# Kernel tuning notes

Measured on AMD Instinct MI355X. Metric: run time of the kernel, lower is better.

## Reference

```python
import jax, jax.numpy as jnp
import numpy as np

ALPHA = 32.0
LN_EPS = 1e-5

def _cdist(a, b):
    # a: [C, M, K], b: [C, N, K] -> [C, M, N] euclidean distances
    d2 = (jnp.sum(a * a, -1)[:, :, None]
          + jnp.sum(b * b, -1)[:, None, :]
          - 2.0 * jnp.einsum('cmk,cnk->cmn', a, b))
    return jnp.sqrt(jnp.maximum(d2, 1e-12))

def setup_inputs() -> dict:
    key = jax.random.key(0)
    k1, k2 = jax.random.split(key)
    B, D, H, W, C = 8, 16, 28, 28, 256
    CN, SS = 128, 28 * 28
    x = jax.random.normal(k1, (B, D, H, W, C), dtype=jnp.float32)
    ln_weight = jnp.ones((C,), dtype=jnp.float32)
    ln_bias = jnp.zeros((C,), dtype=jnp.float32)
    cluster_center = jax.random.uniform(k2, (C, CN, SS), dtype=jnp.float32)
    return {"x": x, "ln_weight": ln_weight, "ln_bias": ln_bias,
            "cluster_center": cluster_center}

def reference(x, ln_weight, ln_bias, cluster_center):
    B, D, H, W, C = x.shape
    CN = cluster_center.shape[1]
    # LayerNorm over last dim (feature_dim)
    mu = jnp.mean(x, -1, keepdims=True)
    var = jnp.mean(jnp.square(x - mu), -1, keepdims=True)
    xn = (x - mu) * jax.lax.rsqrt(var + LN_EPS) * ln_weight + ln_bias
    # B D H W C -> C (B D) (H W)
    x_re = jnp.transpose(xn, (4, 0, 1, 2, 3)).reshape(C, B * D, H * W)
    soft_assign = _cdist(x_re, cluster_center)          # [C, B*D, CN]
    # C (B D) CN -> B D C CN
    x_distance = jnp.transpose(soft_assign.reshape(C, B, D, CN), (1, 2, 0, 3))
    # NegSoftAssign: exp(-alpha*(x - min)) normalized == softmax(-alpha*x)
    x_distance_assign = jax.nn.softmax(-ALPHA * x_distance, axis=-1)
    cluster_dist = _cdist(cluster_center, cluster_center)  # [C, CN, CN]
    return (x_distance, x_distance_assign, cluster_dist)
```

## Files before the change

### kernel.cpp

```cpp
#include <hip/hip_runtime.h>
#include <hip/hip_bf16.h>
#include <math.h>

#define C_DIM 256
#define BD    128
#define HW    784
#define CN    128
#define KPAD  800

typedef short bf16x8 __attribute__((ext_vector_type(8)));
typedef float f32x4 __attribute__((ext_vector_type(4)));

__device__ inline ushort f2b(float f) {
  unsigned u = __float_as_uint(f);
  unsigned r = (u + 0x7FFFu + ((u >> 16) & 1u)) >> 16;
  return (ushort)r;
}

__global__ __launch_bounds__(256) void ln_transpose_kernel(
    const float* __restrict__ x, const float* __restrict__ lnw,
    const float* __restrict__ lnb, ushort* __restrict__ xre,
    float* __restrict__ anorm) {
  const int HT = 56, LD = 257;
  __shared__ float tile[HT * LD];
  __shared__ float sW[256], sB[256];
  __shared__ float nbuf[4][256];
  int t = threadIdx.x, bd = blockIdx.y, hw0 = blockIdx.x * HT;
  sW[t] = lnw[t]; sB[t] = lnb[t];
  const float* xb = x + ((size_t)bd * HW + hw0) * 256;
  for (int r = 0; r < HT; ++r) tile[r * LD + t] = xb[r * 256 + t];
  __syncthreads();
  int w = t >> 6, lane = t & 63;
  float nrm[4] = {0.f, 0.f, 0.f, 0.f};
  for (int r = w; r < HT; r += 4) {
    float v[4]; float s = 0.f;
    for (int j = 0; j < 4; ++j) { v[j] = tile[r * LD + lane + j * 64]; s += v[j]; }
    for (int off = 32; off >= 1; off >>= 1) s += __shfl_xor(s, off, 64);
    float mu = s * (1.0f / 256.0f);
    float s2 = 0.f;
    for (int j = 0; j < 4; ++j) { float dv = v[j] - mu; s2 += dv * dv; }
    for (int off = 32; off >= 1; off >>= 1) s2 += __shfl_xor(s2, off, 64);
    float scale = rsqrtf(s2 * (1.0f / 256.0f) + 1e-5f);
    for (int j = 0; j < 4; ++j) {
      int c = lane + j * 64;
      float y = (v[j] - mu) * scale * sW[c] + sB[c];
      tile[r * LD + c] = y;
      nrm[j] = fmaf(y, y, nrm[j]);
    }
  }
  for (int j = 0; j < 4; ++j) nbuf[w][lane + j * 64] = nrm[j];
  __syncthreads();
  if (lane < HT) {
    for (int i = 0; i < 64; ++i) {
      int c = i * 4 + w;
      xre[(size_t)c * (BD * KPAD) + (size_t)bd * KPAD + hw0 + lane] =
          f2b(tile[lane * LD + c]);
    }
  } else if (blockIdx.x == 13) {
    int p = lane - 56;
    for (int i = 0; i < 64; ++i) {
      int c = i * 4 + w;
      *(ushort2*)(xre + (size_t)c * (BD * KPAD) + (size_t)bd * KPAD + 784 + p * 2) =
          make_ushort2(0, 0);
    }
  }
  float tot = nbuf[0][t] + nbuf[1][t] + nbuf[2][t] + nbuf[3][t];
  atomicAdd(&anorm[t * 128 + bd], tot);
}

__global__ __launch_bounds__(256) void cc_convert_kernel(
    const float* __restrict__ cc, ushort* __restrict__ ccb,
    float* __restrict__ bnorm) {
  int b = blockIdx.x, c = b >> 2;
  int t = threadIdx.x, w = t >> 6, lane = t & 63;
  int r0 = (b & 3) * 32 + w * 8;
  for (int it = 0; it < 8; ++it) {
    int r = r0 + it;
    const float4* src = (const float4*)(cc + ((size_t)c * CN + r) * HW);
    ushort* dst = ccb + (size_t)c * (CN * KPAD) + (size_t)r * KPAD;
    float nrm = 0.f;
    for (int f = lane; f < 196; f += 64) {
      float4 v = src[f];
      nrm = fmaf(v.x, v.x, nrm); nrm = fmaf(v.y, v.y, nrm);
      nrm = fmaf(v.z, v.z, nrm); nrm = fmaf(v.w, v.w, nrm);
      ushort4 o; o.x = f2b(v.x); o.y = f2b(v.y); o.z = f2b(v.z); o.w = f2b(v.w);
      *(ushort4*)(dst + f * 4) = o;
    }
    for (int off = 32; off >= 1; off >>= 1) nrm += __shfl_xor(nrm, off, 64);
    if (lane == 0) bnorm[c * 128 + r] = nrm;
    if (lane < 4) *(ushort4*)(dst + 784 + lane * 4) = make_ushort4(0, 0, 0, 0);
  }
}

__global__ __launch_bounds__(256, 2) void gemm_mfma_kernel(
    const ushort* __restrict__ xre, const ushort* __restrict__ ccb,
    const float* __restrict__ anorm, const float* __restrict__ bnorm,
    float* __restrict__ out_d, float* __restrict__ out_s,
    float* __restrict__ out_c) {
  __shared__ __align__(16) ushort At[512 * 8];
  __shared__ __align__(16) ushort Bt[512 * 8];
  __shared__ float smin[2][128];
  __shared__ float ssum[2][128];
  const int c = blockIdx.x, mode = blockIdx.y;
  const int t = threadIdx.x, w = t >> 6, lane = t & 63;
  const int quad = lane >> 4, ln = lane & 15;
  const int wrow = (w >> 1) * 64, wcol = (w & 1) * 64;
  const ushort* Ag = (mode ? ccb : xre) + (size_t)c * (128 * KPAD);
  const ushort* Bg = ccb + (size_t)c * (128 * KPAD);

  f32x4 acc[4][4];
  for (int i = 0; i < 4; ++i)
    for (int j = 0; j < 4; ++j) acc[i][j] = f32x4{0.f, 0.f, 0.f, 0.f};

  const int ci0 = 128 * w;
  const int row0 = (ci0 + lane) >> 2;
  const int row1 = (ci0 + 64 + lane) >> 2;
  const int q0 = (lane & 3) ^ (row0 & 3);
  const int q1 = (lane & 3) ^ (row1 & 3);
  const ushort* ga0 = Ag + (size_t)row0 * KPAD + q0 * 8;
  const ushort* ga1 = Ag + (size_t)row1 * KPAD + q1 * 8;
  const ushort* gb0 = Bg + (size_t)row0 * KPAD + q0 * 8;
  const ushort* gb1 = Bg + (size_t)row1 * KPAD + q1 * 8;
  ushort* la0 = &At[ci0 * 8];
  ushort* la1 = &At[(ci0 + 64) * 8];
  ushort* lb0 = &Bt[ci0 * 8];
  ushort* lb1 = &Bt[(ci0 + 64) * 8];

  for (int k0 = 0; k0 < 25; ++k0) {
    __syncthreads();
    int kb = k0 * 32;
    __builtin_amdgcn_global_load_lds(
        (const __attribute__((address_space(1))) unsigned int*)(ga0 + kb),
        (__attribute__((address_space(3))) unsigned int*)la0, 16, 0, 0);
    __builtin_amdgcn_global_load_lds(
        (const __attribute__((address_space(1))) unsigned int*)(ga1 + kb),
        (__attribute__((address_space(3))) unsigned int*)la1, 16, 0, 0);
    __builtin_amdgcn_global_load_lds(
        (const __attribute__((address_space(1))) unsigned int*)(gb0 + kb),
        (__attribute__((address_space(3))) unsigned int*)lb0, 16, 0, 0);
    __builtin_amdgcn_global_load_lds(
        (const __attribute__((address_space(1))) unsigned int*)(gb1 + kb),
        (__attribute__((address_space(3))) unsigned int*)lb1, 16, 0, 0);
    __syncthreads();
    bf16x8 af[4], bf[4];
    for (int i = 0; i < 4; ++i) {
      int m = wrow + i * 16 + ln;
      af[i] = *(const bf16x8*)&At[(m * 4 + (quad ^ (m & 3))) * 8];
    }
    for (int j = 0; j < 4; ++j) {
      int n = wcol + j * 16 + ln;
      bf[j] = *(const bf16x8*)&Bt[(n * 4 + (quad ^ (n & 3))) * 8];
    }
    for (int i = 0; i < 4; ++i)
      for (int j = 0; j < 4; ++j)
        acc[i][j] = __builtin_amdgcn_mfma_f32_16x16x32_bf16(af[i], bf[j], acc[i][j], 0, 0, 0);
  }

  const float* rn = (mode ? bnorm : anorm) + c * 128;
  const float* cn = bnorm + c * 128;
  float cnv[4];
  for (int j = 0; j < 4; ++j) cnv[j] = cn[wcol + j * 16 + ln];
  float d[4][4][4];
  for (int i = 0; i < 4; ++i) {
    float rv[4];
    for (int r = 0; r < 4; ++r) rv[r] = rn[wrow + i * 16 + quad * 4 + r];
    for (int j = 0; j < 4; ++j)
      for (int r = 0; r < 4; ++r) {
        float d2 = rv[r] + cnv[j] - 2.f * acc[i][j][r];
        d[i][j][r] = sqrtf(fmaxf(d2, 1e-12f));
      }
  }

  if (mode) {
    float* ob = out_c + (size_t)c * (128 * 128);
    for (int i = 0; i < 4; ++i)
      for (int r = 0; r < 4; ++r) {
        int m = wrow + i * 16 + quad * 4 + r;
        for (int j = 0; j < 4; ++j) ob[m * 128 + wcol + j * 16 + ln] = d[i][j][r];
      }
  } else {
    int half = w & 1;
    for (int i = 0; i < 4; ++i)
      for (int r = 0; r < 4; ++r) {
        int m = wrow + i * 16 + quad * 4 + r;
        size_t ob = ((size_t)m * 256 + c) * 128 + wcol;
        for (int j = 0; j < 4; ++j) out_d[ob + j * 16 + ln] = d[i][j][r];
        float mn = fminf(fminf(d[i][0][r], d[i][1][r]), fminf(d[i][2][r], d[i][3][r]));
        for (int off = 1; off < 16; off <<= 1) mn = fminf(mn, __shfl_xor(mn, off, 64));
        if (ln == 0) smin[half][m] = mn;
      }
    __syncthreads();
    for (int i = 0; i < 4; ++i)
      for (int r = 0; r < 4; ++r) {
        int m = wrow + i * 16 + quad * 4 + r;
        float mn = fminf(smin[0][m], smin[1][m]);
        float s = 0.f;
        for (int j = 0; j < 4; ++j) {
          float e = __expf(-32.f * (d[i][j][r] - mn));
          d[i][j][r] = e;
          s += e;
        }
        for (int off = 1; off < 16; off <<= 1) s += __shfl_xor(s, off, 64);
        if (ln == 0) ssum[half][m] = s;
      }
    __syncthreads();
    for (int i = 0; i < 4; ++i)
      for (int r = 0; r < 4; ++r) {
        int m = wrow + i * 16 + quad * 4 + r;
        float inv = 1.f / (ssum[0][m] + ssum[1][m]);
        size_t ob = ((size_t)m * 256 + c) * 128 + wcol;
        for (int j = 0; j < 4; ++j) out_s[ob + j * 16 + ln] = d[i][j][r] * inv;
      }
  }
}

extern "C" void kernel_launch(void* const* d_in, const int* in_sizes, int n_in,
                              void* d_out, int out_size, void* d_ws, size_t ws_size,
                              hipStream_t stream) {
  const float* x   = (const float*)d_in[0];
  const float* lnw = (const float*)d_in[1];
  const float* lnb = (const float*)d_in[2];
  const float* cc  = (const float*)d_in[3];
  float* out   = (float*)d_out;
  float* out_d = out;
  float* out_s = out + 4194304;
  float* out_c = out + 8388608;

  ushort* xre_b = (ushort*)d_ws;
  ushort* cc_b  = xre_b + 26214400;
  float*  anorm = (float*)(cc_b + 26214400);
  float*  bnorm = anorm + 32768;

  hipMemsetAsync(anorm, 0, 32768 * sizeof(float), stream);
  ln_transpose_kernel<<<dim3(14, 128), 256, 0, stream>>>(x, lnw, lnb, xre_b, anorm);
  cc_convert_kernel<<<1024, 256, 0, stream>>>(cc, cc_b, bnorm);
  gemm_mfma_kernel<<<dim3(256, 2), 256, 0, stream>>>(xre_b, cc_b, anorm, bnorm,
                                                     out_d, out_s, out_c);
}
```

Baseline: 321.9 us.

## Restructure LayerNorm-transpose kernel to compute from registers and stage bf16 tile

The LayerNorm+transpose kernel now reads x directly into registers with float4 loads, normalizes each row through wave shuffles, and writes bf16 results into a transposed shared tile. It then stores packed 32-bit pairs to the global transposed layout. Each block covers 112 spatial positions instead of 56, which halves the grid. This removes the fp32 shared staging pass and the 16-bit scattered global stores. The cost is fewer blocks, 2-way packed LDS writes that may conflict, and changed padding logic.

```diff
diff --git a/kernel.cpp b/kernel.cpp
--- a/kernel.cpp
+++ b/kernel.cpp
@@ -21,51 +21,55 @@
     const float* __restrict__ x, const float* __restrict__ lnw,
     const float* __restrict__ lnb, ushort* __restrict__ xre,
     float* __restrict__ anorm) {
-  const int HT = 56, LD = 257;
-  __shared__ float tile[HT * LD];
-  __shared__ float sW[256], sB[256];
+  __shared__ ushort btile[256 * 114];
   __shared__ float nbuf[4][256];
-  int t = threadIdx.x, bd = blockIdx.y, hw0 = blockIdx.x * HT;
-  sW[t] = lnw[t]; sB[t] = lnb[t];
-  const float* xb = x + ((size_t)bd * HW + hw0) * 256;
-  for (int r = 0; r < HT; ++r) tile[r * LD + t] = xb[r * 256 + t];
+  const int t = threadIdx.x, bd = blockIdx.y, hw0 = blockIdx.x * 112;
+  const int w = t >> 6, lane = t & 63;
+  const int c0 = lane * 4;
+  const float4 wv = *(const float4*)(lnw + c0);
+  const float4 bvv = *(const float4*)(lnb + c0);
+  float nrm[4] = {0.f, 0.f, 0.f, 0.f};
+  const float* xb = x + ((size_t)bd * HW + hw0 + w * 28) * 256;
+  for (int rr = 0; rr < 14; ++rr) {
+    ushort yb[2][4];
+    for (int q = 0; q < 2; ++q) {
+      int r = rr * 2 + q;
+      float4 v = *(const float4*)(xb + (size_t)r * 256 + c0);
+      float s = v.x + v.y + v.z + v.w;
+      for (int off = 32; off >= 1; off >>= 1) s += __shfl_xor(s, off, 64);
+      float mu = s * (1.f / 256.f);
+      float dx = v.x - mu, dy = v.y - mu, dz = v.z - mu, dw = v.w - mu;
+      float s2 = dx * dx + dy * dy + dz * dz + dw * dw;
+      for (int off = 32; off >= 1; off >>= 1) s2 += __shfl_xor(s2, off, 64);
+      float sc = rsqrtf(s2 * (1.f / 256.f) + 1e-5f);
+      float y0 = dx * sc * wv.x + bvv.x;
+      float y1 = dy * sc * wv.y + bvv.y;
+      float y2 = dz * sc * wv.z + bvv.z;
+      float y3 = dw * sc * wv.w + bvv.w;
+      nrm[0] = fmaf(y0, y0, nrm[0]);
+      nrm[1] = fmaf(y1, y1, nrm[1]);
+      nrm[2] = fmaf(y2, y2, nrm[2]);
+      nrm[3] = fmaf(y3, y3, nrm[3]);
+      yb[q][0] = f2b(y0); yb[q][1] = f2b(y1);
+      yb[q][2] = f2b(y2); yb[q][3] = f2b(y3);
+    }
+    int hwl = w * 28 + rr * 2;
+    for (int j = 0; j < 4; ++j)
+      *(ushort2*)&btile[(c0 + j) * 114 + hwl] = make_ushort2(yb[0][j], yb[1][j]);
+  }
+  for (int j = 0; j < 4; ++j) nbuf[w][c0 + j] = nrm[j];
   __syncthreads();
-  int w = t >> 6, lane = t & 63;
-  float nrm[4] = {0.f, 0.f, 0.f, 0.f};
-  for (int r = w; r < HT; r += 4) {
-    float v[4]; float s = 0.f;
-    for (int j = 0; j < 4; ++j) { v[j] = tile[r * LD + lane + j * 64]; s += v[j]; }
-    for (int off = 32; off >= 1; off >>= 1) s += __shfl_xor(s, off, 64);
-    float mu = s * (1.0f / 256.0f);
-    float s2 = 0.f;
-    for (int j = 0; j < 4; ++j) { float dv = v[j] - mu; s2 += dv * dv; }
-    for (int off = 32; off >= 1; off >>= 1) s2 += __shfl_xor(s2, off, 64);
-    float scale = rsqrtf(s2 * (1.0f / 256.0f) + 1e-5f);
-    for (int j = 0; j < 4; ++j) {
-      int c = lane + j * 64;
-      float y = (v[j] - mu) * scale * sW[c] + sB[c];
-      tile[r * LD + c] = y;
-      nrm[j] = fmaf(y, y, nrm[j]);
-    }
-  }
-  for (int j = 0; j < 4; ++j) nbuf[w][lane + j * 64] = nrm[j];
-  __syncthreads();
-  if (lane < HT) {
-    for (int i = 0; i < 64; ++i) {
-      int c = i * 4 + w;
-      xre[(size_t)c * (BD * KPAD) + (size_t)bd * KPAD + hw0 + lane] =
-          f2b(tile[lane * LD + c]);
-    }
-  } else if (blockIdx.x == 13) {
-    int p = lane - 56;
-    for (int i = 0; i < 64; ++i) {
-      int c = i * 4 + w;
-      *(ushort2*)(xre + (size_t)c * (BD * KPAD) + (size_t)bd * KPAD + 784 + p * 2) =
-          make_ushort2(0, 0);
-    }
-  }
   float tot = nbuf[0][t] + nbuf[1][t] + nbuf[2][t] + nbuf[3][t];
   atomicAdd(&anorm[t * 128 + bd], tot);
+  const bool pad = (blockIdx.x == 6) && (lane >= 56);
+  ushort* ob = xre + (size_t)(w * 64) * (BD * KPAD) + (size_t)bd * KPAD + hw0 + lane * 2;
+  for (int i = 0; i < 64; ++i) {
+    int c = w * 64 + i;
+    uint val = 0;
+    if (lane < 56) val = *(const uint*)&btile[c * 114 + lane * 2];
+    if (lane < 56 || pad) *(uint*)ob = val;
+    ob += (size_t)BD * KPAD;
+  }
 }
 
 __global__ __launch_bounds__(256) void cc_convert_kernel(
@@ -232,7 +236,7 @@
   float*  bnorm = anorm + 32768;
 
   hipMemsetAsync(anorm, 0, 32768 * sizeof(float), stream);
-  ln_transpose_kernel<<<dim3(14, 128), 256, 0, stream>>>(x, lnw, lnb, xre_b, anorm);
+  ln_transpose_kernel<<<dim3(7, 128), 256, 0, stream>>>(x, lnw, lnb, xre_b, anorm);
   cc_convert_kernel<<<1024, 256, 0, stream>>>(cc, cc_b, bnorm);
   gemm_mfma_kernel<<<dim3(256, 2), 256, 0, stream>>>(xre_b, cc_b, anorm, bnorm,
                                                      out_d, out_s, out_c);
```

Result: no change. 318.8 us (-1.0%).

## Rewrite LayerNorm-transpose to normalize from registers and stage bf16 tile

Applied to the files above, without the earlier changes.

The LayerNorm+transpose kernel now loads x with float4 loads straight into registers, reduces each row within a 16-lane group, and writes bf16 results into a smaller transposed shared tile instead of staging the fp32 input tile. The global write-out uses 32-bit stores of two bf16 values per lane in 64-wide hw chunks, and the last block handles the 16-row tail plus padding zeros. The grid changes from 14 to 13 blocks per bd. This aims to cut shared-memory traffic and footprint and to widen global stores, at the cost of strided 2-byte shared writes that may cause bank conflicts.

```diff
diff --git a/kernel.cpp b/kernel.cpp
--- a/kernel.cpp
+++ b/kernel.cpp
@@ -21,51 +21,86 @@
     const float* __restrict__ x, const float* __restrict__ lnw,
     const float* __restrict__ lnb, ushort* __restrict__ xre,
     float* __restrict__ anorm) {
-  const int HT = 56, LD = 257;
-  __shared__ float tile[HT * LD];
-  __shared__ float sW[256], sB[256];
+  __shared__ ushort btile[256 * 66];
   __shared__ float nbuf[4][256];
-  int t = threadIdx.x, bd = blockIdx.y, hw0 = blockIdx.x * HT;
-  sW[t] = lnw[t]; sB[t] = lnb[t];
-  const float* xb = x + ((size_t)bd * HW + hw0) * 256;
-  for (int r = 0; r < HT; ++r) tile[r * LD + t] = xb[r * 256 + t];
+  const int t = threadIdx.x, bd = blockIdx.y, bx = blockIdx.x;
+  const int hw0 = bx * 64;
+  const int w = t >> 6, lane = t & 63;
+  const int q = lane >> 4, l = lane & 15;
+  const bool last = (bx == 12);
+  const int ngroups = last ? 1 : 4;
+  const int rpw = ngroups * 4;
+  float4 wv[4], bv[4];
+  for (int s = 0; s < 4; ++s) {
+    wv[s] = *(const float4*)(lnw + s * 64 + l * 4);
+    bv[s] = *(const float4*)(lnb + s * 64 + l * 4);
+  }
+  float nrm[4][4];
+  for (int s = 0; s < 4; ++s)
+    for (int j = 0; j < 4; ++j) nrm[s][j] = 0.f;
+  const float* xb = x + ((size_t)bd * HW + hw0) * 256 + l * 4;
+  for (int g = 0; g < ngroups; ++g) {
+    int r = w * rpw + g * 4 + q;
+    float4 v[4];
+    for (int s = 0; s < 4; ++s)
+      v[s] = *(const float4*)(xb + (size_t)r * 256 + s * 64);
+    float sum = 0.f;
+    for (int s = 0; s < 4; ++s) sum += v[s].x + v[s].y + v[s].z + v[s].w;
+    for (int off = 1; off <= 8; off <<= 1) sum += __shfl_xor(sum, off, 64);
+    float mu = sum * (1.f / 256.f);
+    float var = 0.f;
+    for (int s = 0; s < 4; ++s) {
+      float dx = v[s].x - mu, dy = v[s].y - mu, dz = v[s].z - mu, dw2 = v[s].w - mu;
+      var += dx * dx + dy * dy + dz * dz + dw2 * dw2;
+    }
+    for (int off = 1; off <= 8; off <<= 1) var += __shfl_xor(var, off, 64);
+    float sc = rsqrtf(var * (1.f / 256.f) + 1e-5f);
+    for (int s = 0; s < 4; ++s) {
+      float y0 = (v[s].x - mu) * sc * wv[s].x + bv[s].x;
+      float y1 = (v[s].y - mu) * sc * wv[s].y + bv[s].y;
+      float y2 = (v[s].z - mu) * sc * wv[s].z + bv[s].z;
+      float y3 = (v[s].w - mu) * sc * wv[s].w + bv[s].w;
+      nrm[s][0] = fmaf(y0, y0, nrm[s][0]);
+      nrm[s][1] = fmaf(y1, y1, nrm[s][1]);
+      nrm[s][2] = fmaf(y2, y2, nrm[s][2]);
+      nrm[s][3] = fmaf(y3, y3, nrm[s][3]);
+      int c = s * 64 + l * 4;
+      btile[(c + 0) * 66 + r] = f2b(y0);
+      btile[(c + 1) * 66 + r] = f2b(y1);
+      btile[(c + 2) * 66 + r] = f2b(y2);
+      btile[(c + 3) * 66 + r] = f2b(y3);
+    }
+  }
+  for (int s = 0; s < 4; ++s)
+    for (int j = 0; j < 4; ++j) {
+      float v = nrm[s][j];
+      v += __shfl_xor(v, 16, 64);
+      v += __shfl_xor(v, 32, 64);
+      nrm[s][j] = v;
+    }
+  if (q == 0)
+    for (int s = 0; s < 4; ++s)
+      for (int j = 0; j < 4; ++j) nbuf[w][s * 64 + l * 4 + j] = nrm[s][j];
   __syncthreads();
-  int w = t >> 6, lane = t & 63;
-  float nrm[4] = {0.f, 0.f, 0.f, 0.f};
-  for (int r = w; r < HT; r += 4) {
-    float v[4]; float s = 0.f;
-    for (int j = 0; j < 4; ++j) { v[j] = tile[r * LD + lane + j * 64]; s += v[j]; }
-    for (int off = 32; off >= 1; off >>= 1) s += __shfl_xor(s, off, 64);
-    float mu = s * (1.0f / 256.0f);
-    float s2 = 0.f;
-    for (int j = 0; j < 4; ++j) { float dv = v[j] - mu; s2 += dv * dv; }
-    for (int off = 32; off >= 1; off >>= 1) s2 += __shfl_xor(s2, off, 64);
-    float scale = rsqrtf(s2 * (1.0f / 256.0f) + 1e-5f);
-    for (int j = 0; j < 4; ++j) {
-      int c = lane + j * 64;
-      float y = (v[j] - mu) * scale * sW[c] + sB[c];
-      tile[r * LD + c] = y;
-      nrm[j] = fmaf(y, y, nrm[j]);
-    }
-  }
-  for (int j = 0; j < 4; ++j) nbuf[w][lane + j * 64] = nrm[j];
-  __syncthreads();
-  if (lane < HT) {
-    for (int i = 0; i < 64; ++i) {
-      int c = i * 4 + w;
-      xre[(size_t)c * (BD * KPAD) + (size_t)bd * KPAD + hw0 + lane] =
-          f2b(tile[lane * LD + c]);
-    }
-  } else if (blockIdx.x == 13) {
-    int p = lane - 56;
-    for (int i = 0; i < 64; ++i) {
-      int c = i * 4 + w;
-      *(ushort2*)(xre + (size_t)c * (BD * KPAD) + (size_t)bd * KPAD + 784 + p * 2) =
-          make_ushort2(0, 0);
-    }
-  }
   float tot = nbuf[0][t] + nbuf[1][t] + nbuf[2][t] + nbuf[3][t];
   atomicAdd(&anorm[t * 128 + bd], tot);
+  if (!last) {
+    for (int i = 0; i < 32; ++i) {
+      int c = w * 64 + i * 2 + (lane >> 5);
+      int hwp = (lane & 31) * 2;
+      uint val = *(const uint*)&btile[c * 66 + hwp];
+      *(uint*)(xre + (size_t)c * (BD * KPAD) + (size_t)bd * KPAD + hw0 + hwp) = val;
+    }
+  } else {
+    for (int i = 0; i < 8; ++i) {
+      int c = w * 64 + i * 8 + (lane >> 3);
+      int hwp = (lane & 7) * 2;
+      uint val = *(const uint*)&btile[c * 66 + hwp];
+      ushort* gp = xre + (size_t)c * (BD * KPAD) + (size_t)bd * KPAD + 768;
+      *(uint*)(gp + hwp) = val;
+      *(uint*)(gp + 16 + hwp) = 0u;
+    }
+  }
 }
 
 __global__ __launch_bounds__(256) void cc_convert_kernel(
@@ -232,7 +267,7 @@
   float*  bnorm = anorm + 32768;
 
   hipMemsetAsync(anorm, 0, 32768 * sizeof(float), stream);
-  ln_transpose_kernel<<<dim3(14, 128), 256, 0, stream>>>(x, lnw, lnb, xre_b, anorm);
+  ln_transpose_kernel<<<dim3(13, 128), 256, 0, stream>>>(x, lnw, lnb, xre_b, anorm);
   cc_convert_kernel<<<1024, 256, 0, stream>>>(cc, cc_b, bnorm);
   gemm_mfma_kernel<<<dim3(256, 2), 256, 0, stream>>>(xre_b, cc_b, anorm, bnorm,
                                                      out_d, out_s, out_c);
```

Result: faster. 309.9 us (-3.7%).
